# Performance work log

Hardware: AMD Instinct MI355X
Metric: run time of the kernel (lower is better)

The kernel has to match this reference:

```python
import jax, jax.numpy as jnp
import numpy as np

HEAD_DIM = 128
SCALE = 1.0 / np.sqrt(HEAD_DIM)  # standard 1/sqrt(d) attention scaling


def setup_inputs() -> dict:
    key = jax.random.key(0)
    kq, kk, kv = jax.random.split(key, 3)
    q = jax.random.normal(kq, (2, 32, 2048, HEAD_DIM), dtype=jnp.float16)
    k = jax.random.normal(kk, (2, 8, 2048, HEAD_DIM), dtype=jnp.float16)
    v = jax.random.normal(kv, (2, 8, 2048, HEAD_DIM), dtype=jnp.float16)
    return {"q": q, "k": k, "v": v}


def reference(q, k, v):
    # GQA attention: each of the g = H // KVH query heads in a group attends
    # against the group's single shared K/V head (no K/V duplication).
    b, h, sq, d = q.shape
    kvh = k.shape[1]
    g = h // kvh
    # [b, kvh, g, sq, d] -- group-packed Q, mirroring the kernel's _pack_q
    qg = q.reshape(b, kvh, g, sq, d)
    # fp32 accumulation as in flash-attention kernels
    scores = jnp.einsum(
        'bhgqd,bhkd->bhgqk',
        qg.astype(jnp.float32), k.astype(jnp.float32)) * SCALE
    p = jax.nn.softmax(scores, axis=-1)  # non-causal, full attention
    o = jnp.einsum('bhgqk,bhkd->bhgqd', p, v.astype(jnp.float32))
    return o.reshape(b, h, sq, d).astype(q.dtype)
```

## Files before the change

### kernel.cpp

```cpp
#include <hip/hip_runtime.h>

#define SEQ   2048
#define HD    128
#define BN    64
#define NITER (SEQ / BN)

typedef __fp16 f16x2 __attribute__((ext_vector_type(2)));
typedef __fp16 f16x4 __attribute__((ext_vector_type(4)));
typedef __fp16 f16x8 __attribute__((ext_vector_type(8)));
typedef float  f32x4 __attribute__((ext_vector_type(4)));

__device__ __forceinline__ unsigned pkh(float a, float b) {
  auto h = __builtin_amdgcn_cvt_pkrtz(a, b);
  return __builtin_bit_cast(unsigned, h);
}

__global__ __launch_bounds__(256, 2)
void fa_gqa_kernel(const float* __restrict__ Q,
                   const float* __restrict__ K,
                   const float* __restrict__ V,
                   float* __restrict__ O)
{
  __shared__ unsigned short kt_lds[64 * HD];
  __shared__ unsigned short vt_lds[HD * 64];

  const int tid  = threadIdx.x;
  const int lane = tid & 63;
  const int w    = tid >> 6;
  const int c    = lane & 15;
  const int qh   = lane >> 4;

  const int F     = blockIdx.x;
  const int xcd   = F & 7;
  const int s     = F >> 3;
  const int bh    = xcd * 8 + (s >> 4);
  const int qtile = s & 15;

  const int b = bh >> 5;
  const int h = bh & 31;
  const long qrow0 = (long)bh * SEQ + qtile * 128 + w * 32;
  const float* Qw = Q + qrow0 * HD;
  float*       Ow = O + qrow0 * HD;
  const long kvoff = (long)(b * 8 + (h >> 2)) * SEQ * HD;
  const float* Kb = K + kvoff;
  const float* Vb = V + kvoff;

  f16x8 qf[2][4];
#pragma unroll
  for (int qt = 0; qt < 2; ++qt)
#pragma unroll
    for (int dc = 0; dc < 4; ++dc) {
      const float4* qp = (const float4*)(Qw + (qt * 16 + c) * HD + dc * 32 + qh * 8);
      float4 a = qp[0], bq = qp[1];
      int4 t;
      t.x = (int)pkh(a.x, a.y);
      t.y = (int)pkh(a.z, a.w);
      t.z = (int)pkh(bq.x, bq.y);
      t.w = (int)pkh(bq.z, bq.w);
      qf[qt][dc] = __builtin_bit_cast(f16x8, t);
    }

  f32x4 oacc[2][8];
#pragma unroll
  for (int mt = 0; mt < 2; ++mt)
#pragma unroll
    for (int dt = 0; dt < 8; ++dt)
      oacc[mt][dt] = (f32x4){0.f, 0.f, 0.f, 0.f};

  float mst[2] = {-1e30f, -1e30f};
  float lst[2] = {0.f, 0.f};

  const float K1 = 0.08838834764831845f * 1.4426950408889634f;

  const int krow = tid >> 2;
  const int kq4  = tid & 3;
  const int kq   = tid >> 4;
  const int dc8  = tid & 15;

  for (int it = 0; it < NITER; ++it) {
    const int k0 = it * BN;

    const float* kp = Kb + (long)(k0 + krow) * HD + kq4 * 32;
    int4 ks[4];
#pragma unroll
    for (int jj = 0; jj < 4; ++jj) {
      float4 e = ((const float4*)kp)[2 * jj];
      float4 o = ((const float4*)kp)[2 * jj + 1];
      ks[jj].x = (int)pkh(e.x, e.y);
      ks[jj].y = (int)pkh(e.z, e.w);
      ks[jj].z = (int)pkh(o.x, o.y);
      ks[jj].w = (int)pkh(o.z, o.w);
    }

    const float* vp = Vb + (long)(k0 + 4 * kq) * HD + dc8 * 8;
    float4 vr[4][2];
#pragma unroll
    for (int r = 0; r < 4; ++r) {
      vr[r][0] = ((const float4*)(vp + r * HD))[0];
      vr[r][1] = ((const float4*)(vp + r * HD))[1];
    }
    uint2 vs[8];
#pragma unroll
    for (int jd = 0; jd < 8; ++jd) {
      const int hsel = jd >> 2, e = jd & 3;
      float x0 = ((const float*)&vr[0][hsel])[e];
      float x1 = ((const float*)&vr[1][hsel])[e];
      float x2 = ((const float*)&vr[2][hsel])[e];
      float x3 = ((const float*)&vr[3][hsel])[e];
      vs[jd].x = pkh(x0, x1);
      vs[jd].y = pkh(x2, x3);
    }

    __syncthreads();

#pragma unroll
    for (int jj = 0; jj < 4; ++jj) {
      int j = kq4 * 4 + jj;
      int pos = j ^ (krow & 15);
      *(int4*)(kt_lds + krow * HD + pos * 8) = ks[jj];
    }
#pragma unroll
    for (int jd = 0; jd < 8; ++jd) {
      int d = dc8 * 8 + jd;
      int pos = kq ^ (d & 15) ^ (d >> 4);
      *(uint2*)(vt_lds + d * 64 + pos * 4) = vs[jd];
    }

    __syncthreads();

    f32x4 sacc[4][2];
#pragma unroll
    for (int kt = 0; kt < 4; ++kt)
#pragma unroll
      for (int qt = 0; qt < 2; ++qt)
        sacc[kt][qt] = (f32x4){0.f, 0.f, 0.f, 0.f};

#pragma unroll
    for (int dc = 0; dc < 4; ++dc) {
#pragma unroll
      for (int kt = 0; kt < 4; ++kt) {
        int row = kt * 16 + c;
        int pos = (4 * dc + qh) ^ c;
        f16x8 af = *(const f16x8*)(kt_lds + row * HD + pos * 8);
#pragma unroll
        for (int qt = 0; qt < 2; ++qt)
          sacc[kt][qt] = __builtin_amdgcn_mfma_f32_16x16x32_f16(
              af, qf[qt][dc], sacc[kt][qt], 0, 0, 0);
      }
    }

    float alpha[2];
#pragma unroll
    for (int qt = 0; qt < 2; ++qt) {
      float mx = sacc[0][qt][0];
#pragma unroll
      for (int kt = 0; kt < 4; ++kt)
#pragma unroll
        for (int r = 0; r < 4; ++r)
          mx = fmaxf(mx, sacc[kt][qt][r]);
      mx = fmaxf(mx, __shfl_xor(mx, 16, 64));
      mx = fmaxf(mx, __shfl_xor(mx, 32, 64));
      float mnew = fmaxf(mst[qt], mx);
      alpha[qt] = __builtin_amdgcn_exp2f(K1 * (mst[qt] - mnew));
      mst[qt] = mnew;
      float nm = -K1 * mnew;
      float sum = 0.f;
#pragma unroll
      for (int kt = 0; kt < 4; ++kt)
#pragma unroll
        for (int r = 0; r < 4; ++r) {
          float p = __builtin_amdgcn_exp2f(fmaf(sacc[kt][qt][r], K1, nm));
          sacc[kt][qt][r] = p;
          sum += p;
        }
      lst[qt] = lst[qt] * alpha[qt] + sum;
    }

    f16x4 pf[4][2];
#pragma unroll
    for (int kt = 0; kt < 4; ++kt)
#pragma unroll
      for (int qt = 0; qt < 2; ++qt) {
        uint2 u;
        u.x = pkh(sacc[kt][qt][0], sacc[kt][qt][1]);
        u.y = pkh(sacc[kt][qt][2], sacc[kt][qt][3]);
        pf[kt][qt] = __builtin_bit_cast(f16x4, u);
      }

#pragma unroll
    for (int mt = 0; mt < 2; ++mt)
#pragma unroll
      for (int dt = 0; dt < 8; ++dt)
        oacc[mt][dt] *= alpha[mt];

#pragma unroll
    for (int kt = 0; kt < 4; ++kt) {
#pragma unroll
      for (int dt = 0; dt < 8; ++dt) {
        int pos = (4 * kt + qh) ^ c ^ dt;
        f16x4 vf = *(const f16x4*)(vt_lds + (dt * 16 + c) * 64 + pos * 4);
#pragma unroll
        for (int qt = 0; qt < 2; ++qt)
          oacc[qt][dt] = __builtin_amdgcn_mfma_f32_16x16x16f16(
              vf, pf[kt][qt], oacc[qt][dt], 0, 0, 0);
      }
    }
  }

  float linv[2];
#pragma unroll
  for (int qt = 0; qt < 2; ++qt) {
    float lf = lst[qt];
    lf += __shfl_xor(lf, 16, 64);
    lf += __shfl_xor(lf, 32, 64);
    linv[qt] = 1.0f / lf;
  }
#pragma unroll
  for (int mt = 0; mt < 2; ++mt) {
#pragma unroll
    for (int dt = 0; dt < 8; ++dt) {
      f32x4 ov = oacc[mt][dt] * linv[mt];
      *(f32x4*)(Ow + (mt * 16 + c) * HD + dt * 16 + qh * 4) = ov;
    }
  }
}

extern "C" void kernel_launch(void* const* d_in, const int* in_sizes, int n_in,
                              void* d_out, int out_size, void* d_ws, size_t ws_size,
                              hipStream_t stream) {
  const float* q = (const float*)d_in[0];
  const float* k = (const float*)d_in[1];
  const float* v = (const float*)d_in[2];
  float* o = (float*)d_out;
  fa_gqa_kernel<<<dim3(1024), dim3(256), 0, stream>>>(q, k, v, o);
}
```

Measured before the change: 336.1 us.

## Switch attention MFMAs from 16x16 tiles to 32x32x16 tiles

Recasts both the QK^T and PV matrix products onto 32x32x16 f16 MFMA instructions in place of 16x16x32 and 16x16x16. Each lane now owns one query row, so the softmax reduction needs only one cross-lane shuffle. The V LDS swizzle and fragment layout change to 8-element reads, and P fragments are rearranged through lane shuffles. The aim is fewer MFMA issues, fewer LDS reads and less softmax bookkeeping, at the cost of extra shuffles and selects per iteration and possible register pressure.

```diff
diff --git a/kernel.cpp b/kernel.cpp
--- a/kernel.cpp
+++ b/kernel.cpp
@@ -5,10 +5,9 @@
 #define BN    64
 #define NITER (SEQ / BN)
 
-typedef __fp16 f16x2 __attribute__((ext_vector_type(2)));
-typedef __fp16 f16x4 __attribute__((ext_vector_type(4)));
-typedef __fp16 f16x8 __attribute__((ext_vector_type(8)));
-typedef float  f32x4 __attribute__((ext_vector_type(4)));
+typedef __fp16 f16x8  __attribute__((ext_vector_type(8)));
+typedef float  f32x4  __attribute__((ext_vector_type(4)));
+typedef float  f32x16 __attribute__((ext_vector_type(16)));
 
 __device__ __forceinline__ unsigned pkh(float a, float b) {
   auto h = __builtin_amdgcn_cvt_pkrtz(a, b);
@@ -27,8 +26,9 @@
   const int tid  = threadIdx.x;
   const int lane = tid & 63;
   const int w    = tid >> 6;
-  const int c    = lane & 15;
-  const int qh   = lane >> 4;
+  const int ml   = lane & 31;
+  const int hi   = lane >> 5;
+  const bool hib = (hi != 0);
 
   const int F     = blockIdx.x;
   const int xcd   = F & 7;
@@ -45,30 +45,26 @@
   const float* Kb = K + kvoff;
   const float* Vb = V + kvoff;
 
-  f16x8 qf[2][4];
-#pragma unroll
-  for (int qt = 0; qt < 2; ++qt)
-#pragma unroll
-    for (int dc = 0; dc < 4; ++dc) {
-      const float4* qp = (const float4*)(Qw + (qt * 16 + c) * HD + dc * 32 + qh * 8);
-      float4 a = qp[0], bq = qp[1];
-      int4 t;
-      t.x = (int)pkh(a.x, a.y);
-      t.y = (int)pkh(a.z, a.w);
-      t.z = (int)pkh(bq.x, bq.y);
-      t.w = (int)pkh(bq.z, bq.w);
-      qf[qt][dc] = __builtin_bit_cast(f16x8, t);
-    }
-
-  f32x4 oacc[2][8];
-#pragma unroll
-  for (int mt = 0; mt < 2; ++mt)
-#pragma unroll
-    for (int dt = 0; dt < 8; ++dt)
-      oacc[mt][dt] = (f32x4){0.f, 0.f, 0.f, 0.f};
-
-  float mst[2] = {-1e30f, -1e30f};
-  float lst[2] = {0.f, 0.f};
+  f16x8 qf[8];
+#pragma unroll
+  for (int dc = 0; dc < 8; ++dc) {
+    const float4* qp = (const float4*)(Qw + ml * HD + dc * 16 + hi * 8);
+    float4 a = qp[0], bq = qp[1];
+    int4 t;
+    t.x = (int)pkh(a.x, a.y);
+    t.y = (int)pkh(a.z, a.w);
+    t.z = (int)pkh(bq.x, bq.y);
+    t.w = (int)pkh(bq.z, bq.w);
+    qf[dc] = __builtin_bit_cast(f16x8, t);
+  }
+
+  f32x16 oacc[4];
+#pragma unroll
+  for (int dt = 0; dt < 4; ++dt)
+    oacc[dt] = (f32x16)(0.f);
+
+  float mst = -1e30f;
+  float lst = 0.f;
 
   const float K1 = 0.08838834764831845f * 1.4426950408889634f;
 
@@ -122,105 +118,96 @@
 #pragma unroll
     for (int jd = 0; jd < 8; ++jd) {
       int d = dc8 * 8 + jd;
-      int pos = kq ^ (d & 15) ^ (d >> 4);
-      *(uint2*)(vt_lds + d * 64 + pos * 4) = vs[jd];
+      int sw3 = ((d >> 3) ^ d) & 7;
+      int pos = (kq >> 1) ^ sw3;
+      *(uint2*)(vt_lds + d * 64 + pos * 8 + (kq & 1) * 4) = vs[jd];
     }
 
     __syncthreads();
 
-    f32x4 sacc[4][2];
-#pragma unroll
-    for (int kt = 0; kt < 4; ++kt)
-#pragma unroll
-      for (int qt = 0; qt < 2; ++qt)
-        sacc[kt][qt] = (f32x4){0.f, 0.f, 0.f, 0.f};
-
-#pragma unroll
-    for (int dc = 0; dc < 4; ++dc) {
-#pragma unroll
-      for (int kt = 0; kt < 4; ++kt) {
-        int row = kt * 16 + c;
-        int pos = (4 * dc + qh) ^ c;
+    f32x16 sacc[2];
+    sacc[0] = (f32x16)(0.f);
+    sacc[1] = (f32x16)(0.f);
+
+#pragma unroll
+    for (int dc = 0; dc < 8; ++dc) {
+#pragma unroll
+      for (int kt = 0; kt < 2; ++kt) {
+        int row = kt * 32 + ml;
+        int pos = (2 * dc + hi) ^ (row & 15);
         f16x8 af = *(const f16x8*)(kt_lds + row * HD + pos * 8);
-#pragma unroll
-        for (int qt = 0; qt < 2; ++qt)
-          sacc[kt][qt] = __builtin_amdgcn_mfma_f32_16x16x32_f16(
-              af, qf[qt][dc], sacc[kt][qt], 0, 0, 0);
+        sacc[kt] = __builtin_amdgcn_mfma_f32_32x32x16_f16(
+            af, qf[dc], sacc[kt], 0, 0, 0);
       }
     }
 
-    float alpha[2];
-#pragma unroll
-    for (int qt = 0; qt < 2; ++qt) {
-      float mx = sacc[0][qt][0];
-#pragma unroll
-      for (int kt = 0; kt < 4; ++kt)
-#pragma unroll
-        for (int r = 0; r < 4; ++r)
-          mx = fmaxf(mx, sacc[kt][qt][r]);
-      mx = fmaxf(mx, __shfl_xor(mx, 16, 64));
-      mx = fmaxf(mx, __shfl_xor(mx, 32, 64));
-      float mnew = fmaxf(mst[qt], mx);
-      alpha[qt] = __builtin_amdgcn_exp2f(K1 * (mst[qt] - mnew));
-      mst[qt] = mnew;
-      float nm = -K1 * mnew;
-      float sum = 0.f;
-#pragma unroll
-      for (int kt = 0; kt < 4; ++kt)
-#pragma unroll
-        for (int r = 0; r < 4; ++r) {
-          float p = __builtin_amdgcn_exp2f(fmaf(sacc[kt][qt][r], K1, nm));
-          sacc[kt][qt][r] = p;
-          sum += p;
-        }
-      lst[qt] = lst[qt] * alpha[qt] + sum;
-    }
-
-    f16x4 pf[4][2];
-#pragma unroll
-    for (int kt = 0; kt < 4; ++kt)
-#pragma unroll
-      for (int qt = 0; qt < 2; ++qt) {
-        uint2 u;
-        u.x = pkh(sacc[kt][qt][0], sacc[kt][qt][1]);
-        u.y = pkh(sacc[kt][qt][2], sacc[kt][qt][3]);
-        pf[kt][qt] = __builtin_bit_cast(f16x4, u);
+    float mx = sacc[0][0];
+#pragma unroll
+    for (int kt = 0; kt < 2; ++kt)
+#pragma unroll
+      for (int r = 0; r < 16; ++r)
+        mx = fmaxf(mx, sacc[kt][r]);
+    mx = fmaxf(mx, __shfl_xor(mx, 32, 64));
+    float mnew = fmaxf(mst, mx);
+    float alpha = __builtin_amdgcn_exp2f(K1 * (mst - mnew));
+    mst = mnew;
+    float nm = -K1 * mnew;
+    float sum = 0.f;
+#pragma unroll
+    for (int kt = 0; kt < 2; ++kt)
+#pragma unroll
+      for (int r = 0; r < 16; ++r) {
+        float p = __builtin_amdgcn_exp2f(fmaf(sacc[kt][r], K1, nm));
+        sacc[kt][r] = p;
+        sum += p;
       }
-
-#pragma unroll
-    for (int mt = 0; mt < 2; ++mt)
-#pragma unroll
-      for (int dt = 0; dt < 8; ++dt)
-        oacc[mt][dt] *= alpha[mt];
-
-#pragma unroll
-    for (int kt = 0; kt < 4; ++kt) {
-#pragma unroll
-      for (int dt = 0; dt < 8; ++dt) {
-        int pos = (4 * kt + qh) ^ c ^ dt;
-        f16x4 vf = *(const f16x4*)(vt_lds + (dt * 16 + c) * 64 + pos * 4);
-#pragma unroll
-        for (int qt = 0; qt < 2; ++qt)
-          oacc[qt][dt] = __builtin_amdgcn_mfma_f32_16x16x16f16(
-              vf, pf[kt][qt], oacc[qt][dt], 0, 0, 0);
+    lst = lst * alpha + sum;
+
+#pragma unroll
+    for (int dt = 0; dt < 4; ++dt)
+      oacc[dt] *= alpha;
+
+#pragma unroll
+    for (int st = 0; st < 4; ++st) {
+      const int kt = st >> 1;
+      const int R  = 8 * (st & 1);
+      unsigned pA0 = pkh(sacc[kt][R + 0], sacc[kt][R + 1]);
+      unsigned pA1 = pkh(sacc[kt][R + 2], sacc[kt][R + 3]);
+      unsigned pB0 = pkh(sacc[kt][R + 4], sacc[kt][R + 5]);
+      unsigned pB1 = pkh(sacc[kt][R + 6], sacc[kt][R + 7]);
+      unsigned s0 = hib ? pA0 : pB0;
+      unsigned s1 = hib ? pA1 : pB1;
+      unsigned r0 = (unsigned)__shfl_xor((int)s0, 32, 64);
+      unsigned r1 = (unsigned)__shfl_xor((int)s1, 32, 64);
+      int4 bf;
+      bf.x = (int)(hib ? r0 : pA0);
+      bf.y = (int)(hib ? r1 : pA1);
+      bf.z = (int)(hib ? pB0 : r0);
+      bf.w = (int)(hib ? pB1 : r1);
+      f16x8 pfrag = __builtin_bit_cast(f16x8, bf);
+#pragma unroll
+      for (int dt = 0; dt < 4; ++dt) {
+        int d = dt * 32 + ml;
+        int pos = (2 * st + hi) ^ (((d >> 3) ^ d) & 7);
+        f16x8 vf = *(const f16x8*)(vt_lds + d * 64 + pos * 8);
+        oacc[dt] = __builtin_amdgcn_mfma_f32_32x32x16_f16(
+            vf, pfrag, oacc[dt], 0, 0, 0);
       }
     }
   }
 
-  float linv[2];
-#pragma unroll
-  for (int qt = 0; qt < 2; ++qt) {
-    float lf = lst[qt];
-    lf += __shfl_xor(lf, 16, 64);
-    lf += __shfl_xor(lf, 32, 64);
-    linv[qt] = 1.0f / lf;
-  }
-#pragma unroll
-  for (int mt = 0; mt < 2; ++mt) {
-#pragma unroll
-    for (int dt = 0; dt < 8; ++dt) {
-      f32x4 ov = oacc[mt][dt] * linv[mt];
-      *(f32x4*)(Ow + (mt * 16 + c) * HD + dt * 16 + qh * 4) = ov;
+  float lf = lst + __shfl_xor(lst, 32, 64);
+  float linv = 1.0f / lf;
+#pragma unroll
+  for (int dt = 0; dt < 4; ++dt) {
+#pragma unroll
+    for (int t = 0; t < 4; ++t) {
+      f32x4 ov;
+      ov[0] = oacc[dt][4 * t + 0] * linv;
+      ov[1] = oacc[dt][4 * t + 1] * linv;
+      ov[2] = oacc[dt][4 * t + 2] * linv;
+      ov[3] = oacc[dt][4 * t + 3] * linv;
+      *(f32x4*)(Ow + ml * HD + dt * 32 + 8 * t + 4 * hi) = ov;
     }
   }
 }
```

Result: faster. 321.6 us (-4.3%).
